# Optimization experiments

Hardware: AMD Instinct MI355X
Metric: run time of the kernel (lower is better)

The kernel has to match this reference:

```python
import jax, jax.numpy as jnp
import numpy as np

EPS = np.finfo(np.float32).eps
X_DIM, H_DIM, Z_DIM = 256, 1024, 128
T, B = 128, 256

def _lin(key, fan_in, fan_out):
    k1, k2 = jax.random.split(key)
    lim = 1.0 / np.sqrt(fan_in)
    W = jax.random.uniform(k1, (fan_in, fan_out), jnp.float32, -lim, lim)
    b = jax.random.uniform(k2, (fan_out,), jnp.float32, -lim, lim)
    return W, b

def setup_inputs() -> dict:
    key = jax.random.key(0)
    ks = jax.random.split(key, 20)
    inp = {}
    inp['x'] = jax.random.normal(ks[0], (T, B, X_DIM), jnp.float32)
    inp['h'] = jnp.zeros((1, B, H_DIM), jnp.float32)
    inp['eps'] = jax.random.normal(ks[1], (T, B, Z_DIM), jnp.float32)
    inp['Wpx'], inp['bpx'] = _lin(ks[2], X_DIM, H_DIM)
    inp['Wpz'], inp['bpz'] = _lin(ks[3], Z_DIM, H_DIM)
    inp['Wenc'], inp['benc'] = _lin(ks[4], 2 * H_DIM, H_DIM)
    inp['Wem'], inp['bem'] = _lin(ks[5], H_DIM, Z_DIM)
    inp['Wes'], inp['bes'] = _lin(ks[6], H_DIM, Z_DIM)
    inp['Wpr'], inp['bpr'] = _lin(ks[7], H_DIM, H_DIM)
    inp['Wpm'], inp['bpm'] = _lin(ks[8], H_DIM, Z_DIM)
    inp['Wps'], inp['bps'] = _lin(ks[9], H_DIM, Z_DIM)
    inp['Wdec'], inp['bdec'] = _lin(ks[10], 2 * H_DIM, H_DIM)
    inp['Wdm'], inp['bdm'] = _lin(ks[11], H_DIM, X_DIM)
    inp['Wds'], inp['bds'] = _lin(ks[12], H_DIM, X_DIM)
    # GRU (pytorch layout): W_ih [3H, 2H], W_hh [3H, H]
    lim = 1.0 / np.sqrt(H_DIM)
    inp['W_ih'] = jax.random.uniform(ks[13], (3 * H_DIM, 2 * H_DIM), jnp.float32, -lim, lim)
    inp['W_hh'] = jax.random.uniform(ks[14], (3 * H_DIM, H_DIM), jnp.float32, -lim, lim)
    inp['b_ih'] = jax.random.uniform(ks[15], (3 * H_DIM,), jnp.float32, -lim, lim)
    inp['b_hh'] = jax.random.uniform(ks[16], (3 * H_DIM,), jnp.float32, -lim, lim)
    return inp

def reference(x, h, eps, Wpx, bpx, Wpz, bpz, Wenc, benc, Wem, bem, Wes, bes,
              Wpr, bpr, Wpm, bpm, Wps, bps, Wdec, bdec, Wdm, bdm, Wds, bds,
              W_ih, W_hh, b_ih, b_hh):
    relu = jax.nn.relu
    sp = jax.nn.softplus

    def gru_cell(inp, h_prev):
        gi = inp @ W_ih.T + b_ih          # [B, 3H]
        gh = h_prev @ W_hh.T + b_hh       # [B, 3H]
        i_r, i_z, i_n = jnp.split(gi, 3, axis=-1)
        h_r, h_z, h_n = jnp.split(gh, 3, axis=-1)
        r = jax.nn.sigmoid(i_r + h_r)
        u = jax.nn.sigmoid(i_z + h_z)
        n = jnp.tanh(i_n + r * h_n)
        return (1.0 - u) * n + u * h_prev

    def step(h_t, xe):
        x_t, eps_t = xe
        phi_x_t = relu(x_t @ Wpx + bpx)                               # [B,H]
        enc_t = relu(jnp.concatenate([phi_x_t, h_t], axis=1) @ Wenc + benc)
        enc_mean_t = enc_t @ Wem + bem
        enc_std_t = sp(enc_t @ Wes + bes)
        z_t = enc_mean_t + eps_t * enc_std_t                          # reparam
        phi_z_t = relu(z_t @ Wpz + bpz)
        prior_t = relu(h_t @ Wpr + bpr)
        prior_mean_t = prior_t @ Wpm + bpm
        prior_std_t = sp(prior_t @ Wps + bps)
        dec_t = relu(jnp.concatenate([phi_z_t, h_t], axis=1) @ Wdec + bdec)
        dec_mean_t = dec_t @ Wdm + bdm
        dec_std_t = sp(dec_t @ Wds + bds)
        h_next = gru_cell(jnp.concatenate([phi_x_t, phi_z_t], axis=1), h_t)
        kld_t = 0.5 * jnp.sum(2.0 * jnp.log(prior_std_t + EPS) - 2.0 * jnp.log(enc_std_t + EPS)
                              + (enc_std_t ** 2 + (enc_mean_t - prior_mean_t) ** 2) / prior_std_t ** 2 - 1.0)
        nll_t = jnp.sum(jnp.log(dec_std_t + EPS) + 0.5 * jnp.log(2.0 * jnp.pi)
                        + (x_t - dec_mean_t) ** 2 / (2.0 * dec_std_t ** 2))
        return h_next, (enc_mean_t, enc_std_t, dec_mean_t, dec_std_t, kld_t, nll_t)

    h0 = h[0]  # [B, H]
    _, (enc_means, enc_stds, dec_means, dec_stds, klds, nlls) = jax.lax.scan(step, h0, (x, eps))
    kld_loss = jnp.sum(klds)
    nll_loss = jnp.sum(nlls)
    return (kld_loss, nll_loss, enc_means, enc_stds, dec_means, dec_stds)
```

## Files before the change

kernel.cpp:

```cpp
#include <hip/hip_runtime.h>
#include <math.h>
#include <limits.h>

#define T_DIM 128
#define B_DIM 256
#define X_DIMC 256
#define H_DIMC 1024
#define Z_DIMC 128
#define EPSF 1.1920929e-07f
#define HALF_LOG_2PI 0.91893853320467274f

typedef float f32x4 __attribute__((ext_vector_type(4)));
typedef short bf16x8 __attribute__((ext_vector_type(8)));

struct Seg { int n_end; int kbeg; int kend; const float* bias; int act;
             float* of32; int ld32; short* ob16; int ld16; };
struct Segs { Seg s[4]; };

__device__ __forceinline__ short f2bf(float f) {
    unsigned u = __builtin_bit_cast(unsigned, f);
    u += 0x7fffu + ((u >> 16) & 1u);
    return (short)(u >> 16);
}
__device__ __forceinline__ float act_apply(float x, int act) {
    if (act == 1) return fmaxf(x, 0.f);
    if (act == 2) return x > 0.f ? x + log1pf(expf(-x)) : log1pf(expf(x));
    return x;
}
__device__ __forceinline__ void gload16(const short* g, short* l) {
    __builtin_amdgcn_global_load_lds(
        (const __attribute__((address_space(1))) void*)g,
        (__attribute__((address_space(3))) void*)l, 16, 0, 0);
}

__global__ __launch_bounds__(256) void mmp_k(
    const short* __restrict__ A0, int lda0,
    const short* __restrict__ A1, int lda1,
    const short* __restrict__ A2, int lda2,
    int ks1, int ks2,
    const short* __restrict__ BT, int ldb,
    Segs segs)
{
    __shared__ short As[2][64][32];
    __shared__ short Bs[2][64][32];
    const int tid = threadIdx.x, lane = tid & 63, wid = tid >> 6;
    const int bm0 = blockIdx.x * 64, bn0 = blockIdx.y * 64;
    int si = 0, n0 = 0;
    while (bn0 >= segs.s[si].n_end) { n0 = segs.s[si].n_end; ++si; }
    const Seg sg = segs.s[si];
    const int nit = (sg.kend - sg.kbeg) >> 5;

    const int arow = (wid << 4) + (lane >> 2);
    const int ac8 = (lane & 3) << 3;
    const short* A0r = A0 + (size_t)(bm0 + arow) * lda0;
    const short* A1r = A1 + (size_t)(bm0 + arow) * lda1;
    const short* A2r = A2 + (size_t)(bm0 + arow) * lda2;
    const short* Br  = BT + (size_t)(bn0 + arow) * ldb;

    auto stage = [&](int p, int it) {
        const int gk = sg.kbeg + (it << 5) + ac8;
        const short* ga = (gk < ks1) ? (A0r + gk)
                        : (gk < ks2) ? (A1r + (gk - ks1))
                                     : (A2r + (gk - ks2));
        gload16(ga, &As[p][wid << 4][0]);
        gload16(Br + gk, &Bs[p][wid << 4][0]);
    };

    const int l15 = lane & 15, lg = lane >> 4;
    const int wm = (wid >> 1) << 5, wn = (wid & 1) << 5;
    f32x4 acc[2][2] = {};

    stage(0, 0);
    for (int it = 0; it < nit; ++it) {
        const int p = it & 1;
        if (it + 1 < nit) {
            stage(p ^ 1, it + 1);
            asm volatile("s_waitcnt vmcnt(2)" ::: "memory");
        } else {
            asm volatile("s_waitcnt vmcnt(0)" ::: "memory");
        }
        asm volatile("s_barrier" ::: "memory");
        bf16x8 af0 = *(const bf16x8*)&As[p][wm + l15][lg << 3];
        bf16x8 af1 = *(const bf16x8*)&As[p][wm + 16 + l15][lg << 3];
        bf16x8 bg0 = *(const bf16x8*)&Bs[p][wn + l15][lg << 3];
        bf16x8 bg1 = *(const bf16x8*)&Bs[p][wn + 16 + l15][lg << 3];
        acc[0][0] = __builtin_amdgcn_mfma_f32_16x16x32_bf16(af0, bg0, acc[0][0], 0, 0, 0);
        acc[0][1] = __builtin_amdgcn_mfma_f32_16x16x32_bf16(af0, bg1, acc[0][1], 0, 0, 0);
        acc[1][0] = __builtin_amdgcn_mfma_f32_16x16x32_bf16(af1, bg0, acc[1][0], 0, 0, 0);
        acc[1][1] = __builtin_amdgcn_mfma_f32_16x16x32_bf16(af1, bg1, acc[1][1], 0, 0, 0);
        asm volatile("s_barrier" ::: "memory");
    }

#pragma unroll
    for (int j = 0; j < 2; ++j) {
        const int gn = bn0 + wn + (j << 4) + l15;
        const int cn = gn - n0;
        const float bv = sg.bias[cn];
#pragma unroll
        for (int i = 0; i < 2; ++i) {
            const int gm0 = bm0 + wm + (i << 4) + (lg << 2);
#pragma unroll
            for (int r = 0; r < 4; ++r) {
                float v = act_apply(acc[i][j][r] + bv, sg.act);
                if (sg.of32) sg.of32[(size_t)(gm0 + r) * sg.ld32 + cn] = v;
                if (sg.ob16) sg.ob16[(size_t)(gm0 + r) * sg.ld16 + cn] = f2bf(v);
            }
        }
    }
}

__global__ __launch_bounds__(256) void zmm_k(
    const float* __restrict__ zm, const float* __restrict__ zs,
    const float* __restrict__ ze,
    const short* __restrict__ BT,
    const float* __restrict__ bias, short* __restrict__ outb)
{
    __shared__ short As[64][136];
    __shared__ short Bs[64][136];
    const int tid = threadIdx.x, lane = tid & 63, wid = tid >> 6;
    const int bm0 = blockIdx.x * 64, bn0 = blockIdx.y * 64;
    const int r = tid >> 2, c0 = (tid & 3) << 3;
#pragma unroll
    for (int s = 0; s < 4; ++s) {
        const int col = c0 + s * 32;
        const size_t base = (size_t)(bm0 + r) * 128 + col;
        short tmp[8];
#pragma unroll
        for (int q = 0; q < 8; q += 2) {
            float2 m2 = *(const float2*)(zm + base + q);
            float2 s2 = *(const float2*)(zs + base + q);
            float2 e2 = *(const float2*)(ze + base + q);
            tmp[q]     = f2bf(fmaf(e2.x, s2.x, m2.x));
            tmp[q + 1] = f2bf(fmaf(e2.y, s2.y, m2.y));
        }
        *(bf16x8*)&As[r][col] = *(bf16x8*)tmp;
        *(bf16x8*)&Bs[r][col] = *(const bf16x8*)(BT + (size_t)(bn0 + r) * 128 + col);
    }
    __syncthreads();
    const int l15 = lane & 15, lg = lane >> 4;
    const int wm = (wid >> 1) << 5, wn = (wid & 1) << 5;
    f32x4 acc[2][2] = {};
#pragma unroll
    for (int s = 0; s < 4; ++s) {
        bf16x8 af0 = *(const bf16x8*)&As[wm + l15][(lg << 3) + s * 32];
        bf16x8 af1 = *(const bf16x8*)&As[wm + 16 + l15][(lg << 3) + s * 32];
        bf16x8 bg0 = *(const bf16x8*)&Bs[wn + l15][(lg << 3) + s * 32];
        bf16x8 bg1 = *(const bf16x8*)&Bs[wn + 16 + l15][(lg << 3) + s * 32];
        acc[0][0] = __builtin_amdgcn_mfma_f32_16x16x32_bf16(af0, bg0, acc[0][0], 0, 0, 0);
        acc[0][1] = __builtin_amdgcn_mfma_f32_16x16x32_bf16(af0, bg1, acc[0][1], 0, 0, 0);
        acc[1][0] = __builtin_amdgcn_mfma_f32_16x16x32_bf16(af1, bg0, acc[1][0], 0, 0, 0);
        acc[1][1] = __builtin_amdgcn_mfma_f32_16x16x32_bf16(af1, bg1, acc[1][1], 0, 0, 0);
    }
#pragma unroll
    for (int j = 0; j < 2; ++j) {
        const int gn = bn0 + wn + (j << 4) + l15;
        const float bv = bias[gn];
#pragma unroll
        for (int i = 0; i < 2; ++i) {
            const int gm0 = bm0 + wm + (i << 4) + (lg << 2);
#pragma unroll
            for (int rr = 0; rr < 4; ++rr) {
                float v = fmaxf(acc[i][j][rr] + bv, 0.f);
                outb[(size_t)(gm0 + rr) * 1024 + gn] = f2bf(v);
            }
        }
    }
}

__global__ void packT_k(const float* __restrict__ src, int ldsr,
                        short* __restrict__ dst, int ldd, int n0, int k0)
{
    __shared__ float tile[32][33];
    const int bx = blockIdx.x * 32;
    const int by = blockIdx.y * 32;
    const int tx = threadIdx.x, ty = threadIdx.y;
    for (int i = ty; i < 32; i += 8)
        tile[i][tx] = src[(size_t)(by + i) * ldsr + bx + tx];
    __syncthreads();
    for (int i = ty; i < 32; i += 8)
        dst[(size_t)(n0 + bx + i) * ldd + k0 + by + tx] = f2bf(tile[tx][i]);
}

__global__ void packD_k(const float* __restrict__ src, int ldsr,
                        short* __restrict__ dst, int ldd, int n0, int k0, int kr)
{
    const int idx = blockIdx.x * 256 + threadIdx.x;
    const int n = idx / kr, k = idx % kr;
    dst[(size_t)(n0 + n) * ldd + k0 + k] = f2bf(src[(size_t)n * ldsr + k]);
}

__global__ void cvtx_k(const float* __restrict__ x, short* __restrict__ xb)
{
    const int i = blockIdx.x * 256 + threadIdx.x;
    float4 v = ((const float4*)x)[i];
    short4 s;
    s.x = f2bf(v.x); s.y = f2bf(v.y); s.z = f2bf(v.z); s.w = f2bf(v.w);
    ((short4*)xb)[i] = s;
}

__global__ void hinit_k(const float* __restrict__ h0, float* __restrict__ hf,
                        short* __restrict__ hb)
{
    const int i = blockIdx.x * 256 + threadIdx.x;
    const float v = h0[i];
    hf[i] = v; hb[i] = f2bf(v);
}

__global__ void zero2_k(float* p) { if (threadIdx.x < 2) p[threadIdx.x] = 0.f; }

__global__ void tail_k(const float* __restrict__ gi, const float* __restrict__ gh,
                       const float* __restrict__ h, float* __restrict__ hn,
                       short* __restrict__ hnb,
                       const float* __restrict__ em, const float* __restrict__ es,
                       const float* __restrict__ pm, const float* __restrict__ ps,
                       const float* __restrict__ xt, const float* __restrict__ dm,
                       const float* __restrict__ ds, float* __restrict__ outp)
{
    int bid = blockIdx.x;
    const int tid = threadIdx.x;
    if (bid < (B_DIM * H_DIMC) / 256) {
        const int i = bid * 256 + tid;
        const int b = i >> 10, j = i & (H_DIMC - 1);
        const float* gib = gi + (size_t)b * 3 * H_DIMC;
        const float* ghb = gh + (size_t)b * 3 * H_DIMC;
        const float r = 1.f / (1.f + expf(-(gib[j] + ghb[j])));
        const float u = 1.f / (1.f + expf(-(gib[H_DIMC + j] + ghb[H_DIMC + j])));
        const float n = tanhf(gib[2 * H_DIMC + j] + r * ghb[2 * H_DIMC + j]);
        const float v = (1.f - u) * n + u * h[i];
        hn[i] = v; hnb[i] = f2bf(v);
        return;
    }
    bid -= (B_DIM * H_DIMC) / 256;
    const int KB = (B_DIM * Z_DIMC) / 256;
    float v; int target;
    if (bid < KB) {
        const int i = bid * 256 + tid;
        const float dmn = em[i] - pm[i];
        v = 0.5f * (2.f * logf(ps[i] + EPSF) - 2.f * logf(es[i] + EPSF) +
                    (es[i] * es[i] + dmn * dmn) / (ps[i] * ps[i]) - 1.f);
        target = 0;
    } else {
        const int i = (bid - KB) * 256 + tid;
        const float d = ds[i];
        const float diff = xt[i] - dm[i];
        v = logf(d + EPSF) + HALF_LOG_2PI + diff * diff / (2.f * d * d);
        target = 1;
    }
    for (int o = 32; o > 0; o >>= 1) v += __shfl_down(v, o);
    __shared__ float sred[4];
    if ((tid & 63) == 0) sred[tid >> 6] = v;
    __syncthreads();
    if (tid == 0) atomicAdd(outp + target, sred[0] + sred[1] + sred[2] + sred[3]);
}

static inline Seg seg(int n_end, int kbeg, int kend, const float* bias, int act,
                      float* of32, int ld32, short* ob16, int ld16)
{
    Seg s; s.n_end = n_end; s.kbeg = kbeg; s.kend = kend; s.bias = bias;
    s.act = act; s.of32 = of32; s.ld32 = ld32; s.ob16 = ob16; s.ld16 = ld16;
    return s;
}
static inline Seg segend() { return seg(INT_MAX, 0, 32, nullptr, 0, nullptr, 0, nullptr, 0); }

extern "C" void kernel_launch(void* const* d_in, const int* in_sizes, int n_in,
                              void* d_out_v, int out_size, void* d_ws, size_t ws_size,
                              hipStream_t stream)
{
    (void)in_sizes; (void)n_in; (void)out_size;
    const float* x    = (const float*)d_in[0];
    const float* h0   = (const float*)d_in[1];
    const float* eps  = (const float*)d_in[2];
    const float* Wpx  = (const float*)d_in[3];
    const float* bpx  = (const float*)d_in[4];
    const float* Wpz  = (const float*)d_in[5];
    const float* bpz  = (const float*)d_in[6];
    const float* Wenc = (const float*)d_in[7];
    const float* benc = (const float*)d_in[8];
    const float* Wem  = (const float*)d_in[9];
    const float* bem  = (const float*)d_in[10];
    const float* Wes  = (const float*)d_in[11];
    const float* bes  = (const float*)d_in[12];
    const float* Wpr  = (const float*)d_in[13];
    const float* bpr  = (const float*)d_in[14];
    const float* Wpm  = (const float*)d_in[15];
    const float* bpm  = (const float*)d_in[16];
    const float* Wps  = (const float*)d_in[17];
    const float* bps  = (const float*)d_in[18];
    const float* Wdec = (const float*)d_in[19];
    const float* bdec = (const float*)d_in[20];
    const float* Wdm  = (const float*)d_in[21];
    const float* bdm  = (const float*)d_in[22];
    const float* Wds  = (const float*)d_in[23];
    const float* bds  = (const float*)d_in[24];
    const float* W_ih = (const float*)d_in[25];
    const float* W_hh = (const float*)d_in[26];
    const float* b_ih = (const float*)d_in[27];
    const float* b_hh = (const float*)d_in[28];

    float* out = (float*)d_out_v;
    float* kld_nll   = out;
    float* enc_means = out + 2;
    float* enc_stds  = enc_means + (size_t)T_DIM * B_DIM * Z_DIMC;
    float* dec_means = enc_stds  + (size_t)T_DIM * B_DIM * Z_DIMC;
    float* dec_stds  = dec_means + (size_t)T_DIM * B_DIM * X_DIMC;

    char* wsb = (char*)d_ws;
    size_t off = 0;
    auto takeB = [&](size_t bytes) {
        char* p = wsb + off; off += (bytes + 255) & ~(size_t)255; return p;
    };
    short* WTpx = (short*)takeB((size_t)1024 * 256 * 2);
    short* WT1  = (short*)takeB((size_t)5120 * 2048 * 2);
    short* WT2  = (short*)takeB((size_t)256 * 1024 * 2);
    short* WTpz = (short*)takeB((size_t)1024 * 128 * 2);
    short* WT4  = (short*)takeB((size_t)4096 * 3072 * 2);
    short* WT56 = (short*)takeB((size_t)768 * 2048 * 2);
    short* xb   = (short*)takeB((size_t)T_DIM * B_DIM * X_DIMC * 2);
    float* hf0  = (float*)takeB((size_t)B_DIM * H_DIMC * 4);
    float* hf1  = (float*)takeB((size_t)B_DIM * H_DIMC * 4);
    short* hb0  = (short*)takeB((size_t)B_DIM * H_DIMC * 2);
    short* hb1  = (short*)takeB((size_t)B_DIM * H_DIMC * 2);
    short* enc_b   = (short*)takeB((size_t)B_DIM * H_DIMC * 2);
    short* prior_b = (short*)takeB((size_t)B_DIM * H_DIMC * 2);
    short* phi_zb  = (short*)takeB((size_t)B_DIM * H_DIMC * 2);
    short* dec_b   = (short*)takeB((size_t)B_DIM * H_DIMC * 2);
    float* ghb_ = (float*)takeB((size_t)B_DIM * 3 * H_DIMC * 4);
    float* gib_ = (float*)takeB((size_t)B_DIM * 3 * H_DIMC * 4);
    float* pmb  = (float*)takeB((size_t)B_DIM * Z_DIMC * 4);
    float* psb  = (float*)takeB((size_t)B_DIM * Z_DIMC * 4);
    const size_t phiXb_bytes = (size_t)T_DIM * B_DIM * H_DIMC * 2;
    const bool big = (off + phiXb_bytes) <= ws_size;
    short* phiXb = big ? (short*)takeB(phiXb_bytes) : nullptr;
    short* phiXs = big ? nullptr : (short*)takeB((size_t)B_DIM * H_DIMC * 2);

    const int BIG = 1 << 30;
    const dim3 tb(256), pt(32, 8);

    packT_k<<<dim3(32, 8), pt, 0, stream>>>(Wpx, 1024, WTpx, 256, 0, 0);
    packT_k<<<dim3(32, 64), pt, 0, stream>>>(Wenc, 1024, WT1, 2048, 0, 0);
    packT_k<<<dim3(32, 32), pt, 0, stream>>>(Wpr, 1024, WT1, 2048, 1024, 1024);
    packD_k<<<dim3(3072 * 1024 / 256), tb, 0, stream>>>(W_hh, 1024, WT1, 2048, 2048, 1024, 1024);
    packT_k<<<dim3(4, 32), pt, 0, stream>>>(Wem, 128, WT2, 1024, 0, 0);
    packT_k<<<dim3(4, 32), pt, 0, stream>>>(Wes, 128, WT2, 1024, 128, 0);
    packT_k<<<dim3(32, 4), pt, 0, stream>>>(Wpz, 1024, WTpz, 128, 0, 0);
    packT_k<<<dim3(32, 64), pt, 0, stream>>>(Wdec, 1024, WT4, 3072, 0, 1024);
    packD_k<<<dim3(3072 * 2048 / 256), tb, 0, stream>>>(W_ih, 2048, WT4, 3072, 1024, 0, 2048);
    packT_k<<<dim3(4, 32), pt, 0, stream>>>(Wpm, 128, WT56, 2048, 0, 0);
    packT_k<<<dim3(4, 32), pt, 0, stream>>>(Wps, 128, WT56, 2048, 128, 0);
    packT_k<<<dim3(8, 32), pt, 0, stream>>>(Wdm, 256, WT56, 2048, 256, 1024);
    packT_k<<<dim3(8, 32), pt, 0, stream>>>(Wds, 256, WT56, 2048, 512, 1024);

    cvtx_k<<<dim3((size_t)T_DIM * B_DIM * X_DIMC / 4 / 256), tb, 0, stream>>>(x, xb);
    hinit_k<<<dim3(B_DIM * H_DIMC / 256), tb, 0, stream>>>(h0, hf0, hb0);
    zero2_k<<<1, 64, 0, stream>>>(kld_nll);

    Segs sx;
    sx.s[0] = seg(1024, 0, 256, bpx, 1, nullptr, 0, phiXb ? phiXb : phiXs, 1024);
    sx.s[1] = segend(); sx.s[2] = segend(); sx.s[3] = segend();
    if (big) {
        mm: ;
        mmp_k<<<dim3(T_DIM * B_DIM / 64, 16), tb, 0, stream>>>(
            xb, 256, xb, 256, xb, 256, BIG, BIG, WTpx, 256, sx);
    }

    for (int t = 0; t < T_DIM; ++t) {
        float* hcur = (t & 1) ? hf1 : hf0;
        float* hnxt = (t & 1) ? hf0 : hf1;
        short* hbc  = (t & 1) ? hb1 : hb0;
        short* hbn  = (t & 1) ? hb0 : hb1;
        const short* phiXt = big ? (phiXb + (size_t)t * B_DIM * H_DIMC) : phiXs;
        float* em_t = enc_means + (size_t)t * B_DIM * Z_DIMC;
        float* es_t = enc_stds  + (size_t)t * B_DIM * Z_DIMC;
        float* dm_t = dec_means + (size_t)t * B_DIM * X_DIMC;
        float* ds_t = dec_stds  + (size_t)t * B_DIM * X_DIMC;
        const float* eps_t = eps + (size_t)t * B_DIM * Z_DIMC;
        const float* x_t   = x   + (size_t)t * B_DIM * X_DIMC;

        if (!big) {
            mmp_k<<<dim3(4, 16), tb, 0, stream>>>(
                xb + (size_t)t * B_DIM * X_DIMC, 256,
                xb, 256, xb, 256, BIG, BIG, WTpx, 256, sx);
        }
        Segs g1;
        g1.s[0] = seg(1024, 0, 2048, benc, 1, nullptr, 0, enc_b, 1024);
        g1.s[1] = seg(2048, 1024, 2048, bpr, 1, nullptr, 0, prior_b, 1024);
        g1.s[2] = seg(5120, 1024, 2048, b_hh, 0, ghb_, 3 * H_DIMC, nullptr, 0);
        g1.s[3] = segend();
        mmp_k<<<dim3(4, 80), tb, 0, stream>>>(
            phiXt, 1024, hbc, 1024, hbc, 1024, 1024, BIG, WT1, 2048, g1);
        Segs g2;
        g2.s[0] = seg(128, 0, 1024, bem, 0, em_t, 128, nullptr, 0);
        g2.s[1] = seg(256, 0, 1024, bes, 2, es_t, 128, nullptr, 0);
        g2.s[2] = segend(); g2.s[3] = segend();
        mmp_k<<<dim3(4, 4), tb, 0, stream>>>(
            enc_b, 1024, enc_b, 1024, enc_b, 1024, BIG, BIG, WT2, 1024, g2);
        zmm_k<<<dim3(4, 16), tb, 0, stream>>>(em_t, es_t, eps_t, WTpz, bpz, phi_zb);
        Segs g4;
        g4.s[0] = seg(1024, 1024, 3072, bdec, 1, nullptr, 0, dec_b, 1024);
        g4.s[1] = seg(4096, 0, 2048, b_ih, 0, gib_, 3 * H_DIMC, nullptr, 0);
        g4.s[2] = segend(); g4.s[3] = segend();
        mmp_k<<<dim3(4, 64), tb, 0, stream>>>(
            phiXt, 1024, phi_zb, 1024, hbc, 1024, 1024, 2048, WT4, 3072, g4);
        Segs g5;
        g5.s[0] = seg(128, 0, 1024, bpm, 0, pmb, 128, nullptr, 0);
        g5.s[1] = seg(256, 0, 1024, bps, 2, psb, 128, nullptr, 0);
        g5.s[2] = seg(512, 1024, 2048, bdm, 0, dm_t, 256, nullptr, 0);
        g5.s[3] = seg(768, 1024, 2048, bds, 2, ds_t, 256, nullptr, 0);
        mmp_k<<<dim3(4, 12), tb, 0, stream>>>(
            prior_b, 1024, dec_b, 1024, dec_b, 1024, 1024, BIG, WT56, 2048, g5);
        tail_k<<<dim3(1408), tb, 0, stream>>>(
            gib_, ghb_, hcur, hnxt, hbn,
            em_t, es_t, pmb, psb, x_t, dm_t, ds_t, kld_nll);
    }
}
```

Before: 16.36 ms.

## Fuse GRU/loss tail into GEMM launches and deepen K-tile pipeline with swizzle

Removes the separate per-step tail kernel. The GRU update now runs in extra blocks of the g5 GEMM launch. The loss reduction for the previous step is deferred into extra blocks of the next step's g1 launch, with a final fin_k handling the last step. The GEMM kernel moves from 2 to 3 LDS buffers and from 32 to 64 K per stage, with an XOR swizzle to reduce LDS bank conflicts. This cuts launches and barriers per step. In exchange it raises LDS use per block, and it relies on pmb/psb not being overwritten before the deferred loss reads them: g5 writes them after g1, so the ordering holds.

```diff
diff --git a/kernel.cpp b/kernel.cpp
--- a/kernel.cpp
+++ b/kernel.cpp
@@ -17,6 +17,13 @@
              float* of32; int ld32; short* ob16; int ld16; };
 struct Segs { Seg s[4]; };
 
+struct Extra {
+    const float* gi; const float* gh; const float* h; float* hn; short* hnb;
+    const float* em; const float* es; const float* pm; const float* ps;
+    const float* xt; const float* dm; const float* ds; float* outp;
+    int nby; int enable;
+};
+
 __device__ __forceinline__ short f2bf(float f) {
     unsigned u = __builtin_bit_cast(unsigned, f);
     u += 0x7fffu + ((u >> 16) & 1u);
@@ -33,62 +40,125 @@
         (__attribute__((address_space(3))) void*)l, 16, 0, 0);
 }
 
+__device__ __forceinline__ void gru_body(int bid, int tid, const Extra& ex) {
+    const int i = bid * 256 + tid;
+    const int b = i >> 10, j = i & (H_DIMC - 1);
+    const float* gib = ex.gi + (size_t)b * 3 * H_DIMC;
+    const float* ghb = ex.gh + (size_t)b * 3 * H_DIMC;
+    const float r = 1.f / (1.f + expf(-(gib[j] + ghb[j])));
+    const float u = 1.f / (1.f + expf(-(gib[H_DIMC + j] + ghb[H_DIMC + j])));
+    const float n = tanhf(gib[2 * H_DIMC + j] + r * ghb[2 * H_DIMC + j]);
+    const float v = (1.f - u) * n + u * ex.h[i];
+    ex.hn[i] = v; ex.hnb[i] = f2bf(v);
+}
+
+__device__ __forceinline__ void loss_body(int bid, int tid, const Extra& ex,
+                                          float* sred) {
+    const int KB = (B_DIM * Z_DIMC) / 256;
+    float v; int target;
+    if (bid < KB) {
+        const int i = bid * 256 + tid;
+        const float dmn = ex.em[i] - ex.pm[i];
+        v = 0.5f * (2.f * logf(ex.ps[i] + EPSF) - 2.f * logf(ex.es[i] + EPSF) +
+                    (ex.es[i] * ex.es[i] + dmn * dmn) / (ex.ps[i] * ex.ps[i]) - 1.f);
+        target = 0;
+    } else {
+        const int i = (bid - KB) * 256 + tid;
+        const float d = ex.ds[i];
+        const float diff = ex.xt[i] - ex.dm[i];
+        v = logf(d + EPSF) + HALF_LOG_2PI + diff * diff / (2.f * d * d);
+        target = 1;
+    }
+    for (int o = 32; o > 0; o >>= 1) v += __shfl_down(v, o);
+    if ((tid & 63) == 0) sred[tid >> 6] = v;
+    __syncthreads();
+    if (tid == 0) atomicAdd(ex.outp + target, sred[0] + sred[1] + sred[2] + sred[3]);
+}
+
+template <int EXTRA>
 __global__ __launch_bounds__(256) void mmp_k(
     const short* __restrict__ A0, int lda0,
     const short* __restrict__ A1, int lda1,
     const short* __restrict__ A2, int lda2,
     int ks1, int ks2,
     const short* __restrict__ BT, int ldb,
-    Segs segs)
-{
-    __shared__ short As[2][64][32];
-    __shared__ short Bs[2][64][32];
+    Segs segs, Extra ex)
+{
+    __shared__ short As[3][64][64];
+    __shared__ short Bs[3][64][64];
+    __shared__ float sred[4];
     const int tid = threadIdx.x, lane = tid & 63, wid = tid >> 6;
+    if (EXTRA) {
+        const int by = blockIdx.y;
+        if (by >= ex.nby) {
+            const int bid = (by - ex.nby) * 4 + blockIdx.x;
+            if (EXTRA == 1) gru_body(bid, tid, ex);
+            else if (ex.enable) loss_body(bid, tid, ex, sred);
+            return;
+        }
+    }
     const int bm0 = blockIdx.x * 64, bn0 = blockIdx.y * 64;
     int si = 0, n0 = 0;
     while (bn0 >= segs.s[si].n_end) { n0 = segs.s[si].n_end; ++si; }
     const Seg sg = segs.s[si];
-    const int nit = (sg.kend - sg.kbeg) >> 5;
-
-    const int arow = (wid << 4) + (lane >> 2);
-    const int ac8 = (lane & 3) << 3;
-    const short* A0r = A0 + (size_t)(bm0 + arow) * lda0;
-    const short* A1r = A1 + (size_t)(bm0 + arow) * lda1;
-    const short* A2r = A2 + (size_t)(bm0 + arow) * lda2;
-    const short* Br  = BT + (size_t)(bn0 + arow) * ldb;
+    const int nit = (sg.kend - sg.kbeg) >> 6;
+
+    const int row8 = lane >> 3;
+    const int kc = (((lane & 7) ^ row8) << 3);
+    const int r0 = (wid << 4) + row8, r1 = r0 + 8;
 
     auto stage = [&](int p, int it) {
-        const int gk = sg.kbeg + (it << 5) + ac8;
-        const short* ga = (gk < ks1) ? (A0r + gk)
-                        : (gk < ks2) ? (A1r + (gk - ks1))
-                                     : (A2r + (gk - ks2));
-        gload16(ga, &As[p][wid << 4][0]);
-        gload16(Br + gk, &Bs[p][wid << 4][0]);
+        const int gk = sg.kbeg + (it << 6) + kc;
+        const short* ga0 = (gk < ks1) ? A0 + (size_t)(bm0 + r0) * lda0 + gk
+                         : (gk < ks2) ? A1 + (size_t)(bm0 + r0) * lda1 + (gk - ks1)
+                                      : A2 + (size_t)(bm0 + r0) * lda2 + (gk - ks2);
+        const short* ga1 = (gk < ks1) ? A0 + (size_t)(bm0 + r1) * lda0 + gk
+                         : (gk < ks2) ? A1 + (size_t)(bm0 + r1) * lda1 + (gk - ks1)
+                                      : A2 + (size_t)(bm0 + r1) * lda2 + (gk - ks2);
+        gload16(ga0, &As[p][(wid << 4) + 0][0]);
+        gload16(ga1, &As[p][(wid << 4) + 8][0]);
+        gload16(BT + (size_t)(bn0 + r0) * ldb + gk, &Bs[p][(wid << 4) + 0][0]);
+        gload16(BT + (size_t)(bn0 + r1) * ldb + gk, &Bs[p][(wid << 4) + 8][0]);
     };
 
     const int l15 = lane & 15, lg = lane >> 4;
     const int wm = (wid >> 1) << 5, wn = (wid & 1) << 5;
+    const int swz = (l15 & 7) << 3;
+    const int c0 = (lg << 3) ^ swz;
+    const int c1 = (32 + (lg << 3)) ^ swz;
     f32x4 acc[2][2] = {};
 
     stage(0, 0);
+    if (nit > 1) stage(1, 1);
+    if (nit > 2) stage(2, 2);
+    int p = 0;
     for (int it = 0; it < nit; ++it) {
-        const int p = it & 1;
-        if (it + 1 < nit) {
-            stage(p ^ 1, it + 1);
-            asm volatile("s_waitcnt vmcnt(2)" ::: "memory");
-        } else {
-            asm volatile("s_waitcnt vmcnt(0)" ::: "memory");
-        }
+        const int rem = nit - 1 - it;
+        if (rem >= 2)      asm volatile("s_waitcnt vmcnt(8)" ::: "memory");
+        else if (rem == 1) asm volatile("s_waitcnt vmcnt(4)" ::: "memory");
+        else               asm volatile("s_waitcnt vmcnt(0)" ::: "memory");
         asm volatile("s_barrier" ::: "memory");
-        bf16x8 af0 = *(const bf16x8*)&As[p][wm + l15][lg << 3];
-        bf16x8 af1 = *(const bf16x8*)&As[p][wm + 16 + l15][lg << 3];
-        bf16x8 bg0 = *(const bf16x8*)&Bs[p][wn + l15][lg << 3];
-        bf16x8 bg1 = *(const bf16x8*)&Bs[p][wn + 16 + l15][lg << 3];
-        acc[0][0] = __builtin_amdgcn_mfma_f32_16x16x32_bf16(af0, bg0, acc[0][0], 0, 0, 0);
-        acc[0][1] = __builtin_amdgcn_mfma_f32_16x16x32_bf16(af0, bg1, acc[0][1], 0, 0, 0);
-        acc[1][0] = __builtin_amdgcn_mfma_f32_16x16x32_bf16(af1, bg0, acc[1][0], 0, 0, 0);
-        acc[1][1] = __builtin_amdgcn_mfma_f32_16x16x32_bf16(af1, bg1, acc[1][1], 0, 0, 0);
-        asm volatile("s_barrier" ::: "memory");
+        bf16x8 a00 = *(const bf16x8*)&As[p][wm + l15][c0];
+        bf16x8 a01 = *(const bf16x8*)&As[p][wm + l15][c1];
+        bf16x8 a10 = *(const bf16x8*)&As[p][wm + 16 + l15][c0];
+        bf16x8 a11 = *(const bf16x8*)&As[p][wm + 16 + l15][c1];
+        bf16x8 b00 = *(const bf16x8*)&Bs[p][wn + l15][c0];
+        bf16x8 b01 = *(const bf16x8*)&Bs[p][wn + l15][c1];
+        bf16x8 b10 = *(const bf16x8*)&Bs[p][wn + 16 + l15][c0];
+        bf16x8 b11 = *(const bf16x8*)&Bs[p][wn + 16 + l15][c1];
+        acc[0][0] = __builtin_amdgcn_mfma_f32_16x16x32_bf16(a00, b00, acc[0][0], 0, 0, 0);
+        acc[0][1] = __builtin_amdgcn_mfma_f32_16x16x32_bf16(a00, b10, acc[0][1], 0, 0, 0);
+        acc[1][0] = __builtin_amdgcn_mfma_f32_16x16x32_bf16(a10, b00, acc[1][0], 0, 0, 0);
+        acc[1][1] = __builtin_amdgcn_mfma_f32_16x16x32_bf16(a10, b10, acc[1][1], 0, 0, 0);
+        acc[0][0] = __builtin_amdgcn_mfma_f32_16x16x32_bf16(a01, b01, acc[0][0], 0, 0, 0);
+        acc[0][1] = __builtin_amdgcn_mfma_f32_16x16x32_bf16(a01, b11, acc[0][1], 0, 0, 0);
+        acc[1][0] = __builtin_amdgcn_mfma_f32_16x16x32_bf16(a11, b01, acc[1][0], 0, 0, 0);
+        acc[1][1] = __builtin_amdgcn_mfma_f32_16x16x32_bf16(a11, b11, acc[1][1], 0, 0, 0);
+        if (rem >= 3) {
+            asm volatile("s_waitcnt lgkmcnt(0)\n\ts_barrier" ::: "memory");
+            stage(p, it + 3);
+        }
+        p = (p == 2) ? 0 : p + 1;
     }
 
 #pragma unroll
@@ -208,49 +278,10 @@
 
 __global__ void zero2_k(float* p) { if (threadIdx.x < 2) p[threadIdx.x] = 0.f; }
 
-__global__ void tail_k(const float* __restrict__ gi, const float* __restrict__ gh,
-                       const float* __restrict__ h, float* __restrict__ hn,
-                       short* __restrict__ hnb,
-                       const float* __restrict__ em, const float* __restrict__ es,
-                       const float* __restrict__ pm, const float* __restrict__ ps,
-                       const float* __restrict__ xt, const float* __restrict__ dm,
-                       const float* __restrict__ ds, float* __restrict__ outp)
-{
-    int bid = blockIdx.x;
-    const int tid = threadIdx.x;
-    if (bid < (B_DIM * H_DIMC) / 256) {
-        const int i = bid * 256 + tid;
-        const int b = i >> 10, j = i & (H_DIMC - 1);
-        const float* gib = gi + (size_t)b * 3 * H_DIMC;
-        const float* ghb = gh + (size_t)b * 3 * H_DIMC;
-        const float r = 1.f / (1.f + expf(-(gib[j] + ghb[j])));
-        const float u = 1.f / (1.f + expf(-(gib[H_DIMC + j] + ghb[H_DIMC + j])));
-        const float n = tanhf(gib[2 * H_DIMC + j] + r * ghb[2 * H_DIMC + j]);
-        const float v = (1.f - u) * n + u * h[i];
-        hn[i] = v; hnb[i] = f2bf(v);
-        return;
-    }
-    bid -= (B_DIM * H_DIMC) / 256;
-    const int KB = (B_DIM * Z_DIMC) / 256;
-    float v; int target;
-    if (bid < KB) {
-        const int i = bid * 256 + tid;
-        const float dmn = em[i] - pm[i];
-        v = 0.5f * (2.f * logf(ps[i] + EPSF) - 2.f * logf(es[i] + EPSF) +
-                    (es[i] * es[i] + dmn * dmn) / (ps[i] * ps[i]) - 1.f);
-        target = 0;
-    } else {
-        const int i = (bid - KB) * 256 + tid;
-        const float d = ds[i];
-        const float diff = xt[i] - dm[i];
-        v = logf(d + EPSF) + HALF_LOG_2PI + diff * diff / (2.f * d * d);
-        target = 1;
-    }
-    for (int o = 32; o > 0; o >>= 1) v += __shfl_down(v, o);
+__global__ void fin_k(Extra ex)
+{
     __shared__ float sred[4];
-    if ((tid & 63) == 0) sred[tid >> 6] = v;
-    __syncthreads();
-    if (tid == 0) atomicAdd(outp + target, sred[0] + sred[1] + sred[2] + sred[3]);
+    loss_body(blockIdx.x, threadIdx.x, ex, sred);
 }
 
 static inline Seg seg(int n_end, int kbeg, int kend, const float* bias, int act,
@@ -260,7 +291,7 @@
     s.act = act; s.of32 = of32; s.ld32 = ld32; s.ob16 = ob16; s.ld16 = ld16;
     return s;
 }
-static inline Seg segend() { return seg(INT_MAX, 0, 32, nullptr, 0, nullptr, 0, nullptr, 0); }
+static inline Seg segend() { return seg(INT_MAX, 0, 64, nullptr, 0, nullptr, 0, nullptr, 0); }
 
 extern "C" void kernel_launch(void* const* d_in, const int* in_sizes, int n_in,
                               void* d_out_v, int out_size, void* d_ws, size_t ws_size,
@@ -336,6 +367,9 @@
     const int BIG = 1 << 30;
     const dim3 tb(256), pt(32, 8);
 
+    Extra exnone = {};
+    exnone.nby = INT_MAX;
+
     packT_k<<<dim3(32, 8), pt, 0, stream>>>(Wpx, 1024, WTpx, 256, 0, 0);
     packT_k<<<dim3(32, 64), pt, 0, stream>>>(Wenc, 1024, WT1, 2048, 0, 0);
     packT_k<<<dim3(32, 32), pt, 0, stream>>>(Wpr, 1024, WT1, 2048, 1024, 1024);
@@ -358,9 +392,8 @@
     sx.s[0] = seg(1024, 0, 256, bpx, 1, nullptr, 0, phiXb ? phiXb : phiXs, 1024);
     sx.s[1] = segend(); sx.s[2] = segend(); sx.s[3] = segend();
     if (big) {
-        mm: ;
-        mmp_k<<<dim3(T_DIM * B_DIM / 64, 16), tb, 0, stream>>>(
-            xb, 256, xb, 256, xb, 256, BIG, BIG, WTpx, 256, sx);
+        mmp_k<0><<<dim3(T_DIM * B_DIM / 64, 16), tb, 0, stream>>>(
+            xb, 256, xb, 256, xb, 256, BIG, BIG, WTpx, 256, sx, exnone);
     }
 
     for (int t = 0; t < T_DIM; ++t) {
@@ -377,39 +410,64 @@
         const float* x_t   = x   + (size_t)t * B_DIM * X_DIMC;
 
         if (!big) {
-            mmp_k<<<dim3(4, 16), tb, 0, stream>>>(
+            mmp_k<0><<<dim3(4, 16), tb, 0, stream>>>(
                 xb + (size_t)t * B_DIM * X_DIMC, 256,
-                xb, 256, xb, 256, BIG, BIG, WTpx, 256, sx);
+                xb, 256, xb, 256, BIG, BIG, WTpx, 256, sx, exnone);
         }
         Segs g1;
         g1.s[0] = seg(1024, 0, 2048, benc, 1, nullptr, 0, enc_b, 1024);
         g1.s[1] = seg(2048, 1024, 2048, bpr, 1, nullptr, 0, prior_b, 1024);
         g1.s[2] = seg(5120, 1024, 2048, b_hh, 0, ghb_, 3 * H_DIMC, nullptr, 0);
         g1.s[3] = segend();
-        mmp_k<<<dim3(4, 80), tb, 0, stream>>>(
-            phiXt, 1024, hbc, 1024, hbc, 1024, 1024, BIG, WT1, 2048, g1);
+        {
+            const int tp = (t > 0) ? t - 1 : 0;
+            Extra exl = {};
+            exl.em = enc_means + (size_t)tp * B_DIM * Z_DIMC;
+            exl.es = enc_stds  + (size_t)tp * B_DIM * Z_DIMC;
+            exl.pm = pmb; exl.ps = psb;
+            exl.xt = x + (size_t)tp * B_DIM * X_DIMC;
+            exl.dm = dec_means + (size_t)tp * B_DIM * X_DIMC;
+            exl.ds = dec_stds  + (size_t)tp * B_DIM * X_DIMC;
+            exl.outp = kld_nll; exl.nby = 80; exl.enable = (t > 0);
+            mmp_k<2><<<dim3(4, 176), tb, 0, stream>>>(
+                phiXt, 1024, hbc, 1024, hbc, 1024, 1024, BIG, WT1, 2048, g1, exl);
+        }
         Segs g2;
         g2.s[0] = seg(128, 0, 1024, bem, 0, em_t, 128, nullptr, 0);
         g2.s[1] = seg(256, 0, 1024, bes, 2, es_t, 128, nullptr, 0);
         g2.s[2] = segend(); g2.s[3] = segend();
-        mmp_k<<<dim3(4, 4), tb, 0, stream>>>(
-            enc_b, 1024, enc_b, 1024, enc_b, 1024, BIG, BIG, WT2, 1024, g2);
+        mmp_k<0><<<dim3(4, 4), tb, 0, stream>>>(
+            enc_b, 1024, enc_b, 1024, enc_b, 1024, BIG, BIG, WT2, 1024, g2, exnone);
         zmm_k<<<dim3(4, 16), tb, 0, stream>>>(em_t, es_t, eps_t, WTpz, bpz, phi_zb);
         Segs g4;
         g4.s[0] = seg(1024, 1024, 3072, bdec, 1, nullptr, 0, dec_b, 1024);
         g4.s[1] = seg(4096, 0, 2048, b_ih, 0, gib_, 3 * H_DIMC, nullptr, 0);
         g4.s[2] = segend(); g4.s[3] = segend();
-        mmp_k<<<dim3(4, 64), tb, 0, stream>>>(
-            phiXt, 1024, phi_zb, 1024, hbc, 1024, 1024, 2048, WT4, 3072, g4);
+        mmp_k<0><<<dim3(4, 64), tb, 0, stream>>>(
+            phiXt, 1024, phi_zb, 1024, hbc, 1024, 1024, 2048, WT4, 3072, g4, exnone);
         Segs g5;
         g5.s[0] = seg(128, 0, 1024, bpm, 0, pmb, 128, nullptr, 0);
         g5.s[1] = seg(256, 0, 1024, bps, 2, psb, 128, nullptr, 0);
         g5.s[2] = seg(512, 1024, 2048, bdm, 0, dm_t, 256, nullptr, 0);
         g5.s[3] = seg(768, 1024, 2048, bds, 2, ds_t, 256, nullptr, 0);
-        mmp_k<<<dim3(4, 12), tb, 0, stream>>>(
-            prior_b, 1024, dec_b, 1024, dec_b, 1024, 1024, BIG, WT56, 2048, g5);
-        tail_k<<<dim3(1408), tb, 0, stream>>>(
-            gib_, ghb_, hcur, hnxt, hbn,
-            em_t, es_t, pmb, psb, x_t, dm_t, ds_t, kld_nll);
-    }
-}
+        {
+            Extra exg = {};
+            exg.gi = gib_; exg.gh = ghb_; exg.h = hcur; exg.hn = hnxt; exg.hnb = hbn;
+            exg.nby = 12; exg.enable = 1;
+            mmp_k<1><<<dim3(4, 268), tb, 0, stream>>>(
+                prior_b, 1024, dec_b, 1024, dec_b, 1024, 1024, BIG, WT56, 2048, g5, exg);
+        }
+    }
+    {
+        const int tp = T_DIM - 1;
+        Extra exf = {};
+        exf.em = enc_means + (size_t)tp * B_DIM * Z_DIMC;
+        exf.es = enc_stds  + (size_t)tp * B_DIM * Z_DIMC;
+        exf.pm = pmb; exf.ps = psb;
+        exf.xt = x + (size_t)tp * B_DIM * X_DIMC;
+        exf.dm = dec_means + (size_t)tp * B_DIM * X_DIMC;
+        exf.ds = dec_stds  + (size_t)tp * B_DIM * X_DIMC;
+        exf.outp = kld_nll; exf.nby = 0; exf.enable = 1;
+        fin_k<<<dim3(384), tb, 0, stream>>>(exf);
+    }
+}
```

Result: faster. 14.04 ms (-14.2%).
